# Optimization experiments

Hardware: AMD Instinct MI355X
Metric: run time of the kernel (lower is better)

The kernel has to match this reference:

```python
import jax, jax.numpy as jnp
import numpy as np
from jax import lax

EPS = 1e-6

def _pixel_coords(loc, H, W):
    # normalized [-1,1] xy -> continuous pixel coordinates (x in [.. W-0.5], y likewise)
    wh = jnp.array([W, H], dtype=loc.dtype)
    pos = 0.5 * (jnp.clip(loc, -1.0, 1.0) + 1.0) * wh - 0.5
    return pos[..., 0], pos[..., 1]

def token2map_agg_sparse(x, loc_orig, idx_agg, H, W):
    # scatter token features to the [H,W] map via nearest pixel of each original point,
    # normalized by per-pixel hit count (sparse-matrix formulation in the original).
    B, N, C = x.shape
    N0 = idx_agg.shape[1]
    px, py = _pixel_coords(loc_orig, H, W)
    ix = jnp.clip(jnp.round(px).astype(jnp.int32), 0, W - 1)
    iy = jnp.clip(jnp.round(py).astype(jnp.int32), 0, H - 1)
    idx_hw = (iy * W + ix + jnp.arange(B, dtype=jnp.int32)[:, None] * (H * W)).reshape(-1)
    vals = jnp.take_along_axis(x, idx_agg[..., None].astype(jnp.int32), axis=1)  # [B,N0,C]
    num = jax.ops.segment_sum(vals.reshape(B * N0, C), idx_hw, num_segments=B * H * W)
    cnt = jax.ops.segment_sum(jnp.ones((B * N0,), x.dtype), idx_hw, num_segments=B * H * W)
    fmap = num / (cnt + EPS)[:, None]
    return fmap.reshape(B, H, W, C).transpose(0, 3, 1, 2)  # NCHW

def map2token_agg_mat(fmap, loc_orig, idx_agg, agg_weight, N):
    # bilinear gather at each original point, then weighted aggregation to tokens via idx_agg
    B, C, H, W = fmap.shape
    N0 = idx_agg.shape[1]
    px, py = _pixel_coords(loc_orig, H, W)
    x0 = jnp.clip(jnp.floor(px).astype(jnp.int32), 0, W - 1)
    x1 = jnp.clip(x0 + 1, 0, W - 1)
    y0 = jnp.clip(jnp.floor(py).astype(jnp.int32), 0, H - 1)
    y1 = jnp.clip(y0 + 1, 0, H - 1)
    wx = jnp.minimum(x1.astype(px.dtype), px) - x0.astype(px.dtype)
    wy = jnp.minimum(y1.astype(py.dtype), py) - y0.astype(py.dtype)
    fm = fmap.transpose(0, 2, 3, 1).reshape(B, H * W, C)
    def gather(iy, ix):
        return jnp.take_along_axis(fm, (iy * W + ix)[..., None], axis=1)
    f = ((1 - wx) * (1 - wy))[..., None] * gather(y0, x0) \
      + (wx * (1 - wy))[..., None] * gather(y0, x1) \
      + ((1 - wx) * wy)[..., None] * gather(y1, x0) \
      + (wx * wy)[..., None] * gather(y1, x1)  # [B,N0,C]
    seg = (idx_agg.astype(jnp.int32) + jnp.arange(B, dtype=jnp.int32)[:, None] * N).reshape(-1)
    w = agg_weight.reshape(B * N0)
    wsum = jax.ops.segment_sum(w, seg, num_segments=B * N) + EPS
    wn = w / wsum[seg]
    out = jax.ops.segment_sum(f.reshape(B * N0, C) * wn[:, None], seg, num_segments=B * N)
    return out.reshape(B, N, C)

def dwconv2d(xmap, conv_w, conv_b):
    C = xmap.shape[1]
    y = lax.conv_general_dilated(xmap, conv_w, (1, 1), ((1, 1), (1, 1)),
                                 feature_group_count=C,
                                 dimension_numbers=('NCHW', 'OIHW', 'NCHW'))
    return y + conv_b[None, :, None, None]

def setup_inputs() -> dict:
    key = jax.random.key(0)
    ks = jax.random.split(key, 6)
    B, N, C, N0, H, W = 16, 1536, 768, 3072, 64, 48
    x = jax.random.normal(ks[0], (B, N, C), dtype=jnp.float32)
    loc = jax.random.uniform(ks[1], (B, N, 2), dtype=jnp.float32) * 2.0 - 1.0
    loc_orig = jax.random.uniform(ks[2], (B, N0, 2), dtype=jnp.float32) * 2.0 - 1.0
    idx_agg = jax.random.randint(ks[3], (B, N0), 0, N, dtype=jnp.int32)
    agg_weight = jax.random.uniform(ks[4], (B, N0, 1), dtype=jnp.float32)
    conv_w = jax.random.normal(ks[5], (C, 1, 3, 3), dtype=jnp.float32) * 0.1
    conv_b = jnp.zeros((C,), dtype=jnp.float32)
    return {"x": x, "loc": loc, "loc_orig": loc_orig, "idx_agg": idx_agg,
            "agg_weight": agg_weight, "H": H, "W": W,
            "conv_w": conv_w, "conv_b": conv_b}

def reference(x, loc, loc_orig, idx_agg, agg_weight, H, W, conv_w, conv_b):
    B, N, C = x.shape
    fmap = token2map_agg_sparse(x, loc_orig, idx_agg, H, W)       # [B,C,H,W]
    fmap = dwconv2d(fmap, conv_w, conv_b)                          # depthwise 3x3
    out = map2token_agg_mat(fmap, loc_orig, idx_agg, agg_weight, N)  # [B,N,C]
    return out
```

## Files before the change

kernel.cpp:

```cpp
#include <hip/hip_runtime.h>

#define B_    16
#define N_    1536
#define C_    768
#define N0_   3072
#define H_    64
#define W_    48
#define HW_   (H_ * W_)
#define NPTS  (B_ * N0_)
#define NTOK  (B_ * N_)
#define NPIX  (B_ * HW_)
#define NSCAN (NPIX + NTOK)
#define NBP   (NPIX / 256)
#define NBALL (NSCAN / 256)
#define EPS_  1e-6f
#define TY_   4
#define TX_   8

__global__ void k_wT(const float* __restrict__ w, float* __restrict__ wT) {
    int i = blockIdx.x * blockDim.x + threadIdx.x;
    if (i < C_ * 9) { int c = i / 9, k = i - c * 9; wT[k * C_ + c] = w[i]; }
}

__global__ void k_points(const float* __restrict__ loc_orig,
                         const int* __restrict__ idx_agg,
                         const float* __restrict__ agg_w,
                         int* __restrict__ pixkey, int4* __restrict__ ofs4,
                         float* __restrict__ wxa, float* __restrict__ wya,
                         float* __restrict__ wa,
                         int* __restrict__ cnt_pix, int* __restrict__ cnt_tok,
                         float* __restrict__ wsum) {
    int i = blockIdx.x * blockDim.x + threadIdx.x;
    if (i >= NPTS) return;
    int b = i / N0_;
    float lx = loc_orig[2 * (size_t)i];
    float ly = loc_orig[2 * (size_t)i + 1];
    lx = fminf(fmaxf(lx, -1.f), 1.f);
    ly = fminf(fmaxf(ly, -1.f), 1.f);
    float px = 0.5f * (lx + 1.f) * (float)W_ - 0.5f;
    float py = 0.5f * (ly + 1.f) * (float)H_ - 0.5f;
    int ixn = min(max((int)rintf(px), 0), W_ - 1);
    int iyn = min(max((int)rintf(py), 0), H_ - 1);
    int pk = b * HW_ + iyn * W_ + ixn;
    pixkey[i] = pk;
    int x0 = min(max((int)floorf(px), 0), W_ - 1);
    int x1 = min(x0 + 1, W_ - 1);
    int y0 = min(max((int)floorf(py), 0), H_ - 1);
    int y1 = min(y0 + 1, H_ - 1);
    wxa[i] = fminf((float)x1, px) - (float)x0;
    wya[i] = fminf((float)y1, py) - (float)y0;
    ofs4[i] = make_int4(y0 * W_ + x0, y0 * W_ + x1, y1 * W_ + x0, y1 * W_ + x1);
    float w = agg_w[i];
    wa[i] = w;
    atomicAdd(&cnt_pix[pk], 1);
    int tk = b * N_ + idx_agg[i];
    atomicAdd(&cnt_tok[tk], 1);
    atomicAdd(&wsum[tk], w);
}

__global__ __launch_bounds__(256)
void k_scanA(const int* __restrict__ cnt, int* __restrict__ pre, int* __restrict__ bsum) {
    __shared__ int sh[256];
    int b = blockIdx.x, t = threadIdx.x;
    int i = b * 256 + t;
    int v = cnt[i];
    sh[t] = v;
    __syncthreads();
    for (int d = 1; d < 256; d <<= 1) {
        int x = sh[t];
        int y = (t >= d) ? sh[t - d] : 0;
        __syncthreads();
        sh[t] = x + y;
        __syncthreads();
    }
    pre[i] = sh[t] - v;
    if (t == 255) bsum[b] = sh[255];
}

__global__ __launch_bounds__(256)
void k_scanB(const int* __restrict__ bsum, int* __restrict__ bbase,
             int* __restrict__ off_pix, int* __restrict__ off_tok) {
    __shared__ int sh[256];
    int t = threadIdx.x;
    int v = (t < NBP) ? bsum[t] : 0;
    sh[t] = v;
    __syncthreads();
    for (int d = 1; d < 256; d <<= 1) {
        int x = sh[t];
        int y = (t >= d) ? sh[t - d] : 0;
        __syncthreads();
        sh[t] = x + y;
        __syncthreads();
    }
    if (t < NBP) bbase[t] = sh[t] - v;
    __syncthreads();
    int nbt = NBALL - NBP;
    v = (t < nbt) ? bsum[NBP + t] : 0;
    sh[t] = v;
    __syncthreads();
    for (int d = 1; d < 256; d <<= 1) {
        int x = sh[t];
        int y = (t >= d) ? sh[t - d] : 0;
        __syncthreads();
        sh[t] = x + y;
        __syncthreads();
    }
    if (t < nbt) bbase[NBP + t] = sh[t] - v;
    if (t == 0) { off_pix[NPIX] = NPTS; off_tok[NTOK] = NPTS; }
}

__global__ __launch_bounds__(256)
void k_scanC(const int* __restrict__ pre, const int* __restrict__ bbase,
             int* __restrict__ off_pix, int* __restrict__ cur_pix,
             int* __restrict__ off_tok, int* __restrict__ cur_tok) {
    int b = blockIdx.x, t = threadIdx.x;
    int i = b * 256 + t;
    int val = pre[i] + bbase[b];
    if (b < NBP) { off_pix[i] = val; cur_pix[i] = val; }
    else { int j = i - NPIX; off_tok[j] = val; cur_tok[j] = val; }
}

__global__ void k_fill(const int* __restrict__ pixkey, const int* __restrict__ idx_agg,
                       const float* __restrict__ wxa, const float* __restrict__ wya,
                       const float* __restrict__ wa, const float* __restrict__ wsum,
                       int* __restrict__ cur_pix, int* __restrict__ cur_tok,
                       int* __restrict__ list_pix, int* __restrict__ list_tok,
                       float4* __restrict__ wts4) {
    int i = blockIdx.x * blockDim.x + threadIdx.x;
    if (i >= NPTS) return;
    int b = i / N0_;
    int tok = idx_agg[i];
    int tk = b * N_ + tok;
    int s1 = atomicAdd(&cur_pix[pixkey[i]], 1);
    list_pix[s1] = tk;
    int s2 = atomicAdd(&cur_tok[tk], 1);
    list_tok[s2] = i;
    float wn = wa[i] / (wsum[tk] + EPS_);
    float wx = wxa[i], wy = wya[i];
    wts4[i] = make_float4((1.f - wx) * (1.f - wy) * wn, wx * (1.f - wy) * wn,
                          (1.f - wx) * wy * wn,         wx * wy * wn);
}

template<int CC>
__global__ __launch_bounds__(CC / 4)
void k_scatter(const float4* __restrict__ x4, const int* __restrict__ off_pix,
               const int* __restrict__ list_pix, float4* __restrict__ fmap4,
               int cbase4) {
    int pk = blockIdx.x;
    int t = threadIdx.x;
    int s = off_pix[pk], e = off_pix[pk + 1];
    float4 a = make_float4(0.f, 0.f, 0.f, 0.f);
    for (int j = s; j < e; ++j) {
        int row = list_pix[j];
        float4 v = x4[(size_t)row * (C_ / 4) + cbase4 + t];
        a.x += v.x; a.y += v.y; a.z += v.z; a.w += v.w;
    }
    float sc = 1.f / ((float)(e - s) + EPS_);
    a.x *= sc; a.y *= sc; a.z *= sc; a.w *= sc;
    fmap4[(size_t)pk * (CC / 4) + t] = a;
}

template<int CC>
__global__ __launch_bounds__(CC)
void k_conv(const float* __restrict__ fmap, const float* __restrict__ wT,
            const float* __restrict__ cb, float* __restrict__ out, int cbase) {
    int tile = blockIdx.x;
    int tx0 = (tile % (W_ / TX_)) * TX_;
    int ty0 = (tile / (W_ / TX_)) * TY_;
    int b = blockIdx.y;
    int c = threadIdx.x;
    const float* base = fmap + (size_t)b * HW_ * CC + c;
    float v[TY_ + 2][TX_ + 2];
#pragma unroll
    for (int r = 0; r < TY_ + 2; ++r) {
        int yy = ty0 + r - 1;
        bool yok = (unsigned)yy < (unsigned)H_;
#pragma unroll
        for (int j = 0; j < TX_ + 2; ++j) {
            int xx = tx0 + j - 1;
            bool ok = yok && ((unsigned)xx < (unsigned)W_);
            v[r][j] = ok ? base[(size_t)(yy * W_ + xx) * CC] : 0.f;
        }
    }
    int cg = cbase + c;
    float k0 = wT[0 * C_ + cg], k1 = wT[1 * C_ + cg], k2 = wT[2 * C_ + cg];
    float k3 = wT[3 * C_ + cg], k4 = wT[4 * C_ + cg], k5 = wT[5 * C_ + cg];
    float k6 = wT[6 * C_ + cg], k7 = wT[7 * C_ + cg], k8 = wT[8 * C_ + cg];
    float bias = cb[cg];
    float* ob = out + (size_t)b * HW_ * CC + c;
#pragma unroll
    for (int r = 0; r < TY_; ++r) {
#pragma unroll
        for (int j = 0; j < TX_; ++j) {
            float acc = bias
                + k0 * v[r][j]     + k1 * v[r][j + 1]     + k2 * v[r][j + 2]
                + k3 * v[r + 1][j] + k4 * v[r + 1][j + 1] + k5 * v[r + 1][j + 2]
                + k6 * v[r + 2][j] + k7 * v[r + 2][j + 1] + k8 * v[r + 2][j + 2];
            ob[(size_t)((ty0 + r) * W_ + tx0 + j) * CC] = acc;
        }
    }
}

template<int CC>
__global__ __launch_bounds__(CC / 4)
void k_gather(const float4* __restrict__ conv4, const int* __restrict__ off_tok,
              const int* __restrict__ list_tok, const int4* __restrict__ ofs4,
              const float4* __restrict__ wts4, float4* __restrict__ out4,
              int cbase4) {
    int tk = blockIdx.x;
    int t = threadIdx.x;
    int b = tk / N_;
    int s = off_tok[tk], e = off_tok[tk + 1];
    const float4* bb = conv4 + (size_t)b * HW_ * (CC / 4) + t;
    float4 a = make_float4(0.f, 0.f, 0.f, 0.f);
    for (int j = s; j < e; ++j) {
        int i = list_tok[j];
        int4 o = ofs4[i];
        float4 w = wts4[i];
        float4 p0 = bb[(size_t)o.x * (CC / 4)];
        float4 p1 = bb[(size_t)o.y * (CC / 4)];
        float4 p2 = bb[(size_t)o.z * (CC / 4)];
        float4 p3 = bb[(size_t)o.w * (CC / 4)];
        a.x += w.x * p0.x + w.y * p1.x + w.z * p2.x + w.w * p3.x;
        a.y += w.x * p0.y + w.y * p1.y + w.z * p2.y + w.w * p3.y;
        a.z += w.x * p0.z + w.y * p1.z + w.z * p2.z + w.w * p3.z;
        a.w += w.x * p0.w + w.y * p1.w + w.z * p2.w + w.w * p3.w;
    }
    out4[(size_t)tk * (C_ / 4) + cbase4 + t] = a;
}

template<int CC>
static void run_chunks(const float4* x4, const int* off_pix, const int* list_pix,
                       const int* off_tok, const int* list_tok,
                       const int4* ofs4, const float4* wts4,
                       const float* wT, const float* cb,
                       float* fmap, float* convout, float* out,
                       hipStream_t stream) {
    constexpr int NCH = C_ / CC;
    for (int chunk = 0; chunk < NCH; ++chunk) {
        int cbase = chunk * CC;
        k_scatter<CC><<<B_ * HW_, CC / 4, 0, stream>>>(
            x4, off_pix, list_pix, (float4*)fmap, cbase / 4);
        dim3 gconv((W_ / TX_) * (H_ / TY_), B_);
        k_conv<CC><<<gconv, CC, 0, stream>>>(fmap, wT, cb, convout, cbase);
        k_gather<CC><<<NTOK, CC / 4, 0, stream>>>(
            (const float4*)convout, off_tok, list_tok, ofs4, wts4,
            (float4*)out, cbase / 4);
    }
}

extern "C" void kernel_launch(void* const* d_in, const int* in_sizes, int n_in,
                              void* d_out, int out_size, void* d_ws, size_t ws_size,
                              hipStream_t stream) {
    const float* x        = (const float*)d_in[0];
    const float* loc_orig = (const float*)d_in[2];
    const int*   idx_agg  = (const int*)d_in[3];
    const float* agg_w    = (const float*)d_in[4];
    const float* conv_w   = (const float*)d_in[7];
    const float* conv_b   = (const float*)d_in[8];
    float* out = (float*)d_out;

    char* wsp = (char*)d_ws;
    size_t o = 0;
    auto alloc = [&](size_t bytes) -> void* {
        o = (o + 255) & ~(size_t)255;
        void* p = wsp + o;
        o += bytes;
        return p;
    };
    float*  wT       = (float*)alloc(C_ * 9 * sizeof(float));
    int*    pixkey   = (int*)alloc(NPTS * sizeof(int));
    int4*   ofs4     = (int4*)alloc(NPTS * sizeof(int4));
    float*  wxa      = (float*)alloc(NPTS * sizeof(float));
    float*  wya      = (float*)alloc(NPTS * sizeof(float));
    float*  wa       = (float*)alloc(NPTS * sizeof(float));
    float4* wts4     = (float4*)alloc(NPTS * sizeof(float4));
    int*    cnt_pix  = (int*)alloc((size_t)NSCAN * sizeof(int)
                                   + (size_t)NTOK * sizeof(float));
    int*    cnt_tok  = cnt_pix + NPIX;
    float*  wsum     = (float*)(cnt_tok + NTOK);
    int*    pre      = (int*)alloc((size_t)NSCAN * sizeof(int));
    int*    bsum     = (int*)alloc(NBALL * sizeof(int));
    int*    bbase    = (int*)alloc(NBALL * sizeof(int));
    int*    off_pix  = (int*)alloc((size_t)(NPIX + 1) * sizeof(int));
    int*    off_tok  = (int*)alloc((size_t)(NTOK + 1) * sizeof(int));
    int*    cur_pix  = (int*)alloc((size_t)NPIX * sizeof(int));
    int*    cur_tok  = (int*)alloc((size_t)NTOK * sizeof(int));
    int*    list_pix = (int*)alloc(NPTS * sizeof(int));
    int*    list_tok = (int*)alloc(NPTS * sizeof(int));

    size_t small_end = (o + 255) & ~(size_t)255;
    size_t perchan = (size_t)B_ * HW_ * 2 * sizeof(float);
    size_t avail = (ws_size > small_end + 1024) ? ws_size - small_end - 1024 : 0;
    int cc = 8;
    const int ladder[6] = {384, 256, 128, 64, 32, 16};
    for (int k = 0; k < 6; ++k)
        if (avail >= (size_t)ladder[k] * perchan) { cc = ladder[k]; break; }

    float* fmap    = (float*)alloc((size_t)B_ * HW_ * cc * sizeof(float));
    float* convout = (float*)alloc((size_t)B_ * HW_ * cc * sizeof(float));

    hipMemsetAsync(cnt_pix, 0,
                   (size_t)NSCAN * sizeof(int) + (size_t)NTOK * sizeof(float),
                   stream);

    k_wT<<<(C_ * 9 + 255) / 256, 256, 0, stream>>>(conv_w, wT);
    k_points<<<NPTS / 256, 256, 0, stream>>>(loc_orig, idx_agg, agg_w,
                                             pixkey, ofs4, wxa, wya, wa,
                                             cnt_pix, cnt_tok, wsum);
    k_scanA<<<NBALL, 256, 0, stream>>>(cnt_pix, pre, bsum);
    k_scanB<<<1, 256, 0, stream>>>(bsum, bbase, off_pix, off_tok);
    k_scanC<<<NBALL, 256, 0, stream>>>(pre, bbase, off_pix, cur_pix, off_tok, cur_tok);
    k_fill<<<NPTS / 256, 256, 0, stream>>>(pixkey, idx_agg, wxa, wya, wa, wsum,
                                           cur_pix, cur_tok, list_pix, list_tok, wts4);

    const float4* x4 = (const float4*)x;
    switch (cc) {
        case 384: run_chunks<384>(x4, off_pix, list_pix, off_tok, list_tok, ofs4, wts4,
                                  wT, conv_b, fmap, convout, out, stream); break;
        case 256: run_chunks<256>(x4, off_pix, list_pix, off_tok, list_tok, ofs4, wts4,
                                  wT, conv_b, fmap, convout, out, stream); break;
        case 128: run_chunks<128>(x4, off_pix, list_pix, off_tok, list_tok, ofs4, wts4,
                                  wT, conv_b, fmap, convout, out, stream); break;
        case  64: run_chunks< 64>(x4, off_pix, list_pix, off_tok, list_tok, ofs4, wts4,
                                  wT, conv_b, fmap, convout, out, stream); break;
        case  32: run_chunks< 32>(x4, off_pix, list_pix, off_tok, list_tok, ofs4, wts4,
                                  wT, conv_b, fmap, convout, out, stream); break;
        case  16: run_chunks< 16>(x4, off_pix, list_pix, off_tok, list_tok, ofs4, wts4,
                                  wT, conv_b, fmap, convout, out, stream); break;
        default:  run_chunks<  8>(x4, off_pix, list_pix, off_tok, list_tok, ofs4, wts4,
                                  wT, conv_b, fmap, convout, out, stream); break;
    }
}
```

Baseline: 345.9 us.

## Fuse scatter-average into depthwise conv and swizzle block order

Removes the separate scatter kernel and the fmap intermediate: the conv kernel now computes each pixel's mean of token features on the fly from the per-pixel CSR lists while loading its halo. Both the conv and the gather kernels remap block indices with an interleaving swizzle, and the channel-chunk ladder drops 384 since only convout needs workspace. The fused kernel recomputes halo pixels, roughly 1.9x redundant work for 4x8 tiles, and uses scalar strided loads of x instead of float4, which trades the fmap write and read for more irregular gathers.

Measured after the change: 350.2 us. About the same (+1.2%).

```diff
diff --git a/kernel.cpp b/kernel.cpp
--- a/kernel.cpp
+++ b/kernel.cpp
@@ -16,6 +16,8 @@
 #define EPS_  1e-6f
 #define TY_   4
 #define TX_   8
+#define NTILE ((W_ / TX_) * (H_ / TY_))
+#define NBSC  (B_ * NTILE)
 
 __global__ void k_wT(const float* __restrict__ w, float* __restrict__ wT) {
     int i = blockIdx.x * blockDim.x + threadIdx.x;
@@ -142,34 +144,19 @@
 }
 
 template<int CC>
-__global__ __launch_bounds__(CC / 4)
-void k_scatter(const float4* __restrict__ x4, const int* __restrict__ off_pix,
-               const int* __restrict__ list_pix, float4* __restrict__ fmap4,
-               int cbase4) {
-    int pk = blockIdx.x;
-    int t = threadIdx.x;
-    int s = off_pix[pk], e = off_pix[pk + 1];
-    float4 a = make_float4(0.f, 0.f, 0.f, 0.f);
-    for (int j = s; j < e; ++j) {
-        int row = list_pix[j];
-        float4 v = x4[(size_t)row * (C_ / 4) + cbase4 + t];
-        a.x += v.x; a.y += v.y; a.z += v.z; a.w += v.w;
-    }
-    float sc = 1.f / ((float)(e - s) + EPS_);
-    a.x *= sc; a.y *= sc; a.z *= sc; a.w *= sc;
-    fmap4[(size_t)pk * (CC / 4) + t] = a;
-}
-
-template<int CC>
 __global__ __launch_bounds__(CC)
-void k_conv(const float* __restrict__ fmap, const float* __restrict__ wT,
-            const float* __restrict__ cb, float* __restrict__ out, int cbase) {
-    int tile = blockIdx.x;
+void k_sconv(const float* __restrict__ x, const int* __restrict__ off_pix,
+             const int* __restrict__ list_pix, const float* __restrict__ wT,
+             const float* __restrict__ cb, float* __restrict__ out, int cbase) {
+    int bid = blockIdx.x;
+    int logical = (bid & 7) * (NBSC / 8) + (bid >> 3);
+    int b = logical / NTILE;
+    int tile = logical % NTILE;
     int tx0 = (tile % (W_ / TX_)) * TX_;
     int ty0 = (tile / (W_ / TX_)) * TY_;
-    int b = blockIdx.y;
     int c = threadIdx.x;
-    const float* base = fmap + (size_t)b * HW_ * CC + c;
+    int cg = cbase + c;
+    const float* xb = x + cg;
     float v[TY_ + 2][TX_ + 2];
 #pragma unroll
     for (int r = 0; r < TY_ + 2; ++r) {
@@ -178,11 +165,19 @@
 #pragma unroll
         for (int j = 0; j < TX_ + 2; ++j) {
             int xx = tx0 + j - 1;
-            bool ok = yok && ((unsigned)xx < (unsigned)W_);
-            v[r][j] = ok ? base[(size_t)(yy * W_ + xx) * CC] : 0.f;
+            float acc = 0.f;
+            if (yok && ((unsigned)xx < (unsigned)W_)) {
+                int pk = b * HW_ + yy * W_ + xx;
+                int s = off_pix[pk], e = off_pix[pk + 1];
+                for (int jj = s; jj < e; ++jj) {
+                    int row = list_pix[jj];
+                    acc += xb[(size_t)row * C_];
+                }
+                acc *= 1.f / ((float)(e - s) + EPS_);
+            }
+            v[r][j] = acc;
         }
     }
-    int cg = cbase + c;
     float k0 = wT[0 * C_ + cg], k1 = wT[1 * C_ + cg], k2 = wT[2 * C_ + cg];
     float k3 = wT[3 * C_ + cg], k4 = wT[4 * C_ + cg], k5 = wT[5 * C_ + cg];
     float k6 = wT[6 * C_ + cg], k7 = wT[7 * C_ + cg], k8 = wT[8 * C_ + cg];
@@ -207,7 +202,8 @@
               const int* __restrict__ list_tok, const int4* __restrict__ ofs4,
               const float4* __restrict__ wts4, float4* __restrict__ out4,
               int cbase4) {
-    int tk = blockIdx.x;
+    int bid = blockIdx.x;
+    int tk = (bid & 7) * (NTOK / 8) + (bid >> 3);
     int t = threadIdx.x;
     int b = tk / N_;
     int s = off_tok[tk], e = off_tok[tk + 1];
@@ -230,19 +226,16 @@
 }
 
 template<int CC>
-static void run_chunks(const float4* x4, const int* off_pix, const int* list_pix,
+static void run_chunks(const float* x, const int* off_pix, const int* list_pix,
                        const int* off_tok, const int* list_tok,
                        const int4* ofs4, const float4* wts4,
                        const float* wT, const float* cb,
-                       float* fmap, float* convout, float* out,
-                       hipStream_t stream) {
+                       float* convout, float* out, hipStream_t stream) {
     constexpr int NCH = C_ / CC;
     for (int chunk = 0; chunk < NCH; ++chunk) {
         int cbase = chunk * CC;
-        k_scatter<CC><<<B_ * HW_, CC / 4, 0, stream>>>(
-            x4, off_pix, list_pix, (float4*)fmap, cbase / 4);
-        dim3 gconv((W_ / TX_) * (H_ / TY_), B_);
-        k_conv<CC><<<gconv, CC, 0, stream>>>(fmap, wT, cb, convout, cbase);
+        k_sconv<CC><<<NBSC, CC, 0, stream>>>(x, off_pix, list_pix, wT, cb,
+                                             convout, cbase);
         k_gather<CC><<<NTOK, CC / 4, 0, stream>>>(
             (const float4*)convout, off_tok, list_tok, ofs4, wts4,
             (float4*)out, cbase / 4);
@@ -290,14 +283,13 @@
     int*    list_tok = (int*)alloc(NPTS * sizeof(int));
 
     size_t small_end = (o + 255) & ~(size_t)255;
-    size_t perchan = (size_t)B_ * HW_ * 2 * sizeof(float);
+    size_t perchan = (size_t)B_ * HW_ * sizeof(float);
     size_t avail = (ws_size > small_end + 1024) ? ws_size - small_end - 1024 : 0;
     int cc = 8;
-    const int ladder[6] = {384, 256, 128, 64, 32, 16};
-    for (int k = 0; k < 6; ++k)
+    const int ladder[5] = {256, 128, 64, 32, 16};
+    for (int k = 0; k < 5; ++k)
         if (avail >= (size_t)ladder[k] * perchan) { cc = ladder[k]; break; }
 
-    float* fmap    = (float*)alloc((size_t)B_ * HW_ * cc * sizeof(float));
     float* convout = (float*)alloc((size_t)B_ * HW_ * cc * sizeof(float));
 
     hipMemsetAsync(cnt_pix, 0,
@@ -314,21 +306,18 @@
     k_fill<<<NPTS / 256, 256, 0, stream>>>(pixkey, idx_agg, wxa, wya, wa, wsum,
                                            cur_pix, cur_tok, list_pix, list_tok, wts4);
 
-    const float4* x4 = (const float4*)x;
     switch (cc) {
-        case 384: run_chunks<384>(x4, off_pix, list_pix, off_tok, list_tok, ofs4, wts4,
-                                  wT, conv_b, fmap, convout, out, stream); break;
-        case 256: run_chunks<256>(x4, off_pix, list_pix, off_tok, list_tok, ofs4, wts4,
-                                  wT, conv_b, fmap, convout, out, stream); break;
-        case 128: run_chunks<128>(x4, off_pix, list_pix, off_tok, list_tok, ofs4, wts4,
-                                  wT, conv_b, fmap, convout, out, stream); break;
-        case  64: run_chunks< 64>(x4, off_pix, list_pix, off_tok, list_tok, ofs4, wts4,
-                                  wT, conv_b, fmap, convout, out, stream); break;
-        case  32: run_chunks< 32>(x4, off_pix, list_pix, off_tok, list_tok, ofs4, wts4,
-                                  wT, conv_b, fmap, convout, out, stream); break;
-        case  16: run_chunks< 16>(x4, off_pix, list_pix, off_tok, list_tok, ofs4, wts4,
-                                  wT, conv_b, fmap, convout, out, stream); break;
-        default:  run_chunks<  8>(x4, off_pix, list_pix, off_tok, list_tok, ofs4, wts4,
-                                  wT, conv_b, fmap, convout, out, stream); break;
-    }
-}
+        case 256: run_chunks<256>(x, off_pix, list_pix, off_tok, list_tok, ofs4, wts4,
+                                  wT, conv_b, convout, out, stream); break;
+        case 128: run_chunks<128>(x, off_pix, list_pix, off_tok, list_tok, ofs4, wts4,
+                                  wT, conv_b, convout, out, stream); break;
+        case  64: run_chunks< 64>(x, off_pix, list_pix, off_tok, list_tok, ofs4, wts4,
+                                  wT, conv_b, convout, out, stream); break;
+        case  32: run_chunks< 32>(x, off_pix, list_pix, off_tok, list_tok, ofs4, wts4,
+                                  wT, conv_b, convout, out, stream); break;
+        case  16: run_chunks< 16>(x, off_pix, list_pix, off_tok, list_tok, ofs4, wts4,
+                                  wT, conv_b, convout, out, stream); break;
+        default:  run_chunks<  8>(x, off_pix, list_pix, off_tok, list_tok, ofs4, wts4,
+                                  wT, conv_b, convout, out, stream); break;
+    }
+}
```
